# Kernel tuning notes

Hardware: AMD Instinct MI355X
Metric: run time of the kernel (lower is better)

The kernel has to match this reference:

```python
import jax, jax.numpy as jnp
import numpy as np

N_PROTS = 2048
MOLS_PER_PROT = 8
N_MOLS = N_PROTS * MOLS_PER_PROT
DIM = 768
MARGIN = 0.5


def setup_inputs() -> dict:
    key = jax.random.key(0)
    k1, k2, k3 = jax.random.split(key, 3)
    prot_emb = jax.random.normal(k1, (N_PROTS, DIM), dtype=jnp.float32)
    mol_emb = jax.random.normal(k2, (N_MOLS, DIM), dtype=jnp.float32)
    # L2-normalize like typical CLIP-style retrieval embeddings
    prot_emb = prot_emb / jnp.linalg.norm(prot_emb, axis=1, keepdims=True)
    mol_emb = mol_emb / jnp.linalg.norm(mol_emb, axis=1, keepdims=True)
    # block-structured labels: protein i paired with mols [8i, 8i+8)
    rows = jnp.repeat(jnp.arange(N_PROTS), MOLS_PER_PROT)
    cols = jnp.arange(N_MOLS)
    labels = jnp.zeros((N_PROTS, N_MOLS), dtype=jnp.float32).at[rows, cols].set(1.0)
    # pIC50 values in [2, 10]
    pic50_matrix = 2.0 + 8.0 * jax.random.uniform(k3, (N_PROTS, N_MOLS), dtype=jnp.float32)
    logit_scale = jnp.float32(1.0 / 0.07)
    return {"prot_emb": prot_emb, "mol_emb": mol_emb, "labels": labels,
            "pic50_matrix": pic50_matrix, "logit_scale": logit_scale}


def reference(prot_emb, mol_emb, labels, pic50_matrix, logit_scale):
    n_prots = prot_emb.shape[0]
    n_mols = mol_emb.shape[0]
    sim = jnp.matmul(prot_emb, mol_emb.T) * logit_scale  # [n_prots, n_mols]

    # affinity-weighted InfoNCE (prot -> mol)
    pic50_norm = jnp.clip((pic50_matrix - 2.0) / 8.0, 0.0, 1.0)
    pos_w = labels * pic50_norm
    pos_w = pos_w / (pos_w.sum(axis=1, keepdims=True) + 1e-8)
    loss_p2m = -jnp.sum(pos_w * jax.nn.log_softmax(sim, axis=1)) / n_prots

    # mol -> prot NLL
    mol_labels = jnp.argmax(labels, axis=0)  # [n_mols]
    lsm_m2p = jax.nn.log_softmax(sim.T, axis=1)  # [n_mols, n_prots]
    loss_m2p = -jnp.mean(lsm_m2p[jnp.arange(n_mols), mol_labels])

    # pairwise margin-ranking among positives (exactly MOLS_PER_PROT positives per protein)
    P = MOLS_PER_PROT
    _, pos_idx = jax.lax.top_k(labels, P)  # [n_prots, P] indices of positives
    pos_pic = jnp.take_along_axis(pic50_matrix, pos_idx, axis=1)  # [n_prots, P]
    pos_sc = jnp.take_along_axis(sim, pos_idx, axis=1)            # [n_prots, P]
    dp = pos_pic[:, :, None] - pos_pic[:, None, :]  # [n_prots, P, P]
    ds = pos_sc[:, :, None] - pos_sc[:, None, :]
    pair = jnp.where(dp > 0, jax.nn.relu(MARGIN - ds),
                     jnp.where(dp < 0, jax.nn.relu(MARGIN + ds), 0.0))
    upper = jnp.triu(jnp.ones((P, P), dtype=bool), k=1)  # unordered pairs j<k
    n_pairs = n_prots * (P * (P - 1) // 2)
    ranking_loss = jnp.sum(jnp.where(upper[None], pair, 0.0)) / n_pairs

    # negative push-down
    neg_loss = jnp.mean(jax.nn.relu(sim * (1.0 - labels)))

    total = loss_p2m + loss_m2p + 0.5 * ranking_loss + 0.1 * neg_loss
    return (total, loss_p2m, loss_m2p, ranking_loss, neg_loss)
```

## Files before the change

### kernel.cpp

```cpp
#include <hip/hip_runtime.h>
#include <hip/hip_bf16.h>
#include <math.h>

#define N_PROTS 2048
#define N_MOLS  16384
#define DIM     768
#define SHIFT   16.0f
#define MARGIN  0.5f

typedef __attribute__((ext_vector_type(8))) short short8;
typedef __attribute__((ext_vector_type(4))) float f32x4;
typedef __attribute__((ext_vector_type(4))) unsigned short us4;
typedef __attribute__((ext_vector_type(8))) unsigned short us8;

__device__ __forceinline__ unsigned short bf16rnd(float x) {
    unsigned int u = __float_as_uint(x);
    u += 0x7fffu + ((u >> 16) & 1u);
    return (unsigned short)(u >> 16);
}

__device__ __forceinline__ void gload16(const void* g, void* l) {
    __builtin_amdgcn_global_load_lds(
        (const __attribute__((address_space(1))) unsigned int*)g,
        (__attribute__((address_space(3))) unsigned int*)l, 16, 0, 0);
}

__device__ __forceinline__ int sig4(int x) { return (x + (x >> 2)) & 3; }

#define ACC_FLOATS 34824
#define PROT_BF_OFF_B 139296ull
#define PROT_BF_BYTES (2048ull*768*2)
#define MOL_BF_OFF_B  (PROT_BF_OFF_B + PROT_BF_BYTES)
#define MOL_BF_BYTES  (16384ull*768*2)
#define WS_NEED       (MOL_BF_OFF_B + MOL_BF_BYTES)

__global__ __launch_bounds__(256)
void convert_bf16(const float* __restrict__ prot, const float* __restrict__ mol,
                  unsigned short* __restrict__ protBf, unsigned short* __restrict__ molBf,
                  float* __restrict__ wsZero)
{
    const size_t PROT_G = (size_t)N_PROTS * DIM / 8;
    size_t t = (size_t)blockIdx.x * 256 + threadIdx.x;
    if (t < (ACC_FLOATS + 3) / 4) {
        float4 z = {0.f, 0.f, 0.f, 0.f};
        ((float4*)wsZero)[t] = z;
    }
    const float* src;
    unsigned short* dst;
    if (t < PROT_G) { src = prot + t * 8; dst = protBf + t * 8; }
    else            { size_t u = t - PROT_G; src = mol + u * 8; dst = molBf + u * 8; }
    float4 v0 = ((const float4*)src)[0];
    float4 v1 = ((const float4*)src)[1];
    us8 o;
    o[0] = bf16rnd(v0.x); o[1] = bf16rnd(v0.y); o[2] = bf16rnd(v0.z); o[3] = bf16rnd(v0.w);
    o[4] = bf16rnd(v1.x); o[5] = bf16rnd(v1.y); o[6] = bf16rnd(v1.z); o[7] = bf16rnd(v1.w);
    *(us8*)dst = o;
}

__global__ __launch_bounds__(512)
void sim_pass_bf16_v4(const unsigned short* __restrict__ protBf,
                      const unsigned short* __restrict__ molBf,
                      const float* __restrict__ scale_p,
                      float* __restrict__ row_se, float* __restrict__ col_se,
                      float* __restrict__ pos_sim, float* __restrict__ scalars)
{
    __shared__ unsigned short As[4][256][32];
    __shared__ unsigned short Bs[4][256][32];
    __shared__ float redBuf[8];

    const int tid = threadIdx.x;
    const int bid  = blockIdx.x;
    const int xcd  = bid & 7;
    const int sl8  = bid >> 3;
    const int bx   = xcd * 8 + (sl8 & 7);
    const int by   = sl8 >> 3;
    const int rowBase = by * 256;
    const int colBase = bx * 256;

    const int wave = tid >> 6;
    const int lane = tid & 63;
    const int wm = wave >> 2;
    const int wn = wave & 3;
    const int l15 = lane & 15;
    const int q   = lane >> 4;

    const int rsub = lane >> 2;
    const int cs   = lane & 3;
    const int csrc = (cs ^ sig4(rsub)) << 3;
    const unsigned short* aP =
        protBf + (size_t)(rowBase + wave * 32 + rsub) * DIM + csrc;
    const unsigned short* bP =
        molBf  + (size_t)(colBase + wave * 32 + rsub) * DIM + csrc;

#define STAGE_A(sl, ptr) do { \
    gload16((ptr),                     &As[sl][wave * 32][0]);      \
    gload16((ptr) + (size_t)16 * DIM,  &As[sl][wave * 32 + 16][0]); \
} while (0)
#define STAGE_B(sl, ptr) do { \
    gload16((ptr),                     &Bs[sl][wave * 32][0]);      \
    gload16((ptr) + (size_t)16 * DIM,  &Bs[sl][wave * 32 + 16][0]); \
} while (0)

    f32x4 acc[8][4];
#pragma unroll
    for (int i = 0; i < 8; ++i)
#pragma unroll
        for (int j = 0; j < 4; ++j) acc[i][j] = (f32x4){0.f, 0.f, 0.f, 0.f};

    STAGE_A(0, aP);      STAGE_B(0, bP);
    STAGE_A(1, aP + 32); STAGE_B(1, bP + 32);
    STAGE_A(2, aP + 64); STAGE_B(2, bP + 64);

    const int fArow = wm * 128 + l15;
    const int fBrow = wn * 64 + l15;
    const int fsw   = (q ^ sig4(l15)) << 3;

#pragma unroll 1
    for (int t = 0; t < 24; ++t) {
        const int sl = t & 3;
        const int pf = (t + 3) & 3;
        const int kt = (t < 21) ? (t + 3) : (t - 5);
        const unsigned short* aPt = aP + (size_t)kt * 32;
        const unsigned short* bPt = bP + (size_t)kt * 32;

        asm volatile("s_waitcnt vmcnt(8)" ::: "memory");
        __builtin_amdgcn_s_barrier();
        __builtin_amdgcn_sched_barrier(0);

        short8 aF[4], bF[4];
#pragma unroll
        for (int ni = 0; ni < 4; ++ni)
            bF[ni] = *(const short8*)&Bs[sl][fBrow + ni * 16][fsw];
#pragma unroll
        for (int mi = 0; mi < 4; ++mi)
            aF[mi] = *(const short8*)&As[sl][fArow + mi * 16][fsw];
        STAGE_A(pf, aPt);
        __builtin_amdgcn_s_setprio(1);
#pragma unroll
        for (int mi = 0; mi < 4; ++mi)
#pragma unroll
            for (int ni = 0; ni < 4; ++ni)
                acc[mi][ni] = __builtin_amdgcn_mfma_f32_16x16x32_bf16(
                    aF[mi], bF[ni], acc[mi][ni], 0, 0, 0);
        __builtin_amdgcn_s_setprio(0);

#pragma unroll
        for (int mi = 0; mi < 4; ++mi)
            aF[mi] = *(const short8*)&As[sl][fArow + 64 + mi * 16][fsw];
        STAGE_B(pf, bPt);
        __builtin_amdgcn_s_setprio(1);
#pragma unroll
        for (int mi = 0; mi < 4; ++mi)
#pragma unroll
            for (int ni = 0; ni < 4; ++ni)
                acc[4 + mi][ni] = __builtin_amdgcn_mfma_f32_16x16x32_bf16(
                    aF[mi], bF[ni], acc[4 + mi][ni], 0, 0, 0);
        __builtin_amdgcn_s_setprio(0);
    }
    asm volatile("s_waitcnt vmcnt(0)" ::: "memory");
#undef STAGE_A
#undef STAGE_B

    const float scale = scale_p[0];
    float csum[4] = {0.f, 0.f, 0.f, 0.f};
    float rl = 0.f;
#pragma unroll
    for (int mi = 0; mi < 8; ++mi) {
        float rs[4] = {0.f, 0.f, 0.f, 0.f};
#pragma unroll
        for (int ni = 0; ni < 4; ++ni) {
#pragma unroll
            for (int r = 0; r < 4; ++r) {
                float sim = acc[mi][ni][r] * scale;
                float e = __expf(sim - SHIFT);
                rs[r] += e;
                csum[ni] += e;
                rl += fmaxf(sim, 0.f);
                int rg = rowBase + wm * 128 + mi * 16 + q * 4 + r;
                int cg = colBase + wn * 64 + ni * 16 + l15;
                if ((cg >> 3) == rg) pos_sim[cg] = sim;
            }
        }
#pragma unroll
        for (int r = 0; r < 4; ++r) {
            float v = rs[r];
            v += __shfl_xor(v, 1); v += __shfl_xor(v, 2);
            v += __shfl_xor(v, 4); v += __shfl_xor(v, 8);
            if (l15 == 0)
                atomicAdd(&row_se[rowBase + wm * 128 + mi * 16 + q * 4 + r], v);
        }
    }
#pragma unroll
    for (int ni = 0; ni < 4; ++ni) {
        float v = csum[ni];
        v += __shfl_xor(v, 16); v += __shfl_xor(v, 32);
        if (q == 0)
            atomicAdd(&col_se[colBase + wn * 64 + ni * 16 + l15], v);
    }
#pragma unroll
    for (int m = 1; m < 64; m <<= 1) rl += __shfl_xor(rl, m);
    if (lane == 0) redBuf[wave] = rl;
    __syncthreads();
    if (tid == 0) {
        float sv = 0.f;
#pragma unroll
        for (int w = 0; w < 8; ++w) sv += redBuf[w];
        atomicAdd(&scalars[0], sv);
    }
}

__global__ __launch_bounds__(256, 2)
void sim_pass(const float* __restrict__ prot, const float* __restrict__ mol,
              const float* __restrict__ scale_p,
              float* __restrict__ row_se, float* __restrict__ col_se,
              float* __restrict__ pos_sim, float* __restrict__ scalars)
{
    __shared__ unsigned short As[128][32];
    __shared__ unsigned short Bs[128][32];
    __shared__ float redBuf[4];

    const int tid = threadIdx.x;
    const int rowBase = blockIdx.y * 128;
    const int colBase = blockIdx.x * 128;
    const int wave = tid >> 6;
    const int lane = tid & 63;
    const int wr = (wave >> 1) * 64;
    const int wc = (wave & 1) * 64;
    const int l15 = lane & 15;
    const int q   = lane >> 4;

    f32x4 acc[4][4];
#pragma unroll
    for (int i = 0; i < 4; ++i)
#pragma unroll
        for (int j = 0; j < 4; ++j) acc[i][j] = (f32x4){0.f, 0.f, 0.f, 0.f};

    const float* aBase = prot + (size_t)rowBase * DIM;
    const float* bBase = mol  + (size_t)colBase * DIM;
    float4 aReg[4], bReg[4];
#pragma unroll
    for (int i = 0; i < 4; ++i) {
        int f = tid + 256 * i;
        int row = f >> 3, c4 = f & 7;
        aReg[i] = *(const float4*)(aBase + (size_t)row * DIM + (c4 << 2));
        bReg[i] = *(const float4*)(bBase + (size_t)row * DIM + (c4 << 2));
    }
#pragma unroll 1
    for (int s = 0; s < DIM / 32; ++s) {
#pragma unroll
        for (int i = 0; i < 4; ++i) {
            int f = tid + 256 * i;
            int row = f >> 3, c4 = f & 7;
            us4 av, bv;
            av.x = bf16rnd(aReg[i].x); av.y = bf16rnd(aReg[i].y);
            av.z = bf16rnd(aReg[i].z); av.w = bf16rnd(aReg[i].w);
            bv.x = bf16rnd(bReg[i].x); bv.y = bf16rnd(bReg[i].y);
            bv.z = bf16rnd(bReg[i].z); bv.w = bf16rnd(bReg[i].w);
            *(us4*)&As[row][c4 << 2] = av;
            *(us4*)&Bs[row][c4 << 2] = bv;
        }
        __syncthreads();
        if (s + 1 < DIM / 32) {
            int k0 = (s + 1) * 32;
#pragma unroll
            for (int i = 0; i < 4; ++i) {
                int f = tid + 256 * i;
                int row = f >> 3, c4 = f & 7;
                aReg[i] = *(const float4*)(aBase + (size_t)row * DIM + k0 + (c4 << 2));
                bReg[i] = *(const float4*)(bBase + (size_t)row * DIM + k0 + (c4 << 2));
            }
        }
        short8 aF[4], bF[4];
#pragma unroll
        for (int mi = 0; mi < 4; ++mi) aF[mi] = *(const short8*)&As[wr + mi * 16 + l15][q * 8];
#pragma unroll
        for (int ni = 0; ni < 4; ++ni) bF[ni] = *(const short8*)&Bs[wc + ni * 16 + l15][q * 8];
#pragma unroll
        for (int mi = 0; mi < 4; ++mi)
#pragma unroll
            for (int ni = 0; ni < 4; ++ni)
                acc[mi][ni] = __builtin_amdgcn_mfma_f32_16x16x32_bf16(aF[mi], bF[ni], acc[mi][ni], 0, 0, 0);
        __syncthreads();
    }

    const float scale = scale_p[0];
    float rsum[4][4];
    float csum[4] = {0.f, 0.f, 0.f, 0.f};
    float rl = 0.f;
#pragma unroll
    for (int mi = 0; mi < 4; ++mi)
#pragma unroll
        for (int r = 0; r < 4; ++r) rsum[mi][r] = 0.f;
#pragma unroll
    for (int mi = 0; mi < 4; ++mi) {
#pragma unroll
        for (int ni = 0; ni < 4; ++ni) {
#pragma unroll
            for (int r = 0; r < 4; ++r) {
                float sim = acc[mi][ni][r] * scale;
                float e = __expf(sim - SHIFT);
                rsum[mi][r] += e;
                csum[ni] += e;
                rl += fmaxf(sim, 0.f);
                int rg = rowBase + wr + mi * 16 + q * 4 + r;
                int cg = colBase + wc + ni * 16 + l15;
                if ((cg >> 3) == rg) pos_sim[cg] = sim;
            }
        }
    }
#pragma unroll
    for (int mi = 0; mi < 4; ++mi) {
#pragma unroll
        for (int r = 0; r < 4; ++r) {
            float v = rsum[mi][r];
            v += __shfl_xor(v, 1); v += __shfl_xor(v, 2);
            v += __shfl_xor(v, 4); v += __shfl_xor(v, 8);
            if (l15 == 0)
                atomicAdd(&row_se[rowBase + wr + mi * 16 + q * 4 + r], v);
        }
    }
#pragma unroll
    for (int ni = 0; ni < 4; ++ni) {
        float v = csum[ni];
        v += __shfl_xor(v, 16); v += __shfl_xor(v, 32);
        if (q == 0)
            atomicAdd(&col_se[colBase + wc + ni * 16 + l15], v);
    }
#pragma unroll
    for (int m = 1; m < 64; m <<= 1) rl += __shfl_xor(rl, m);
    if (lane == 0) redBuf[wave] = rl;
    __syncthreads();
    if (tid == 0)
        atomicAdd(&scalars[0], redBuf[0] + redBuf[1] + redBuf[2] + redBuf[3]);
}

__global__ __launch_bounds__(256)
void finalize_mb(const float* __restrict__ row_se, const float* __restrict__ col_se,
                 const float* __restrict__ pos_sim, const float* __restrict__ pic50,
                 float* __restrict__ scalars, float* __restrict__ out)
{
    int j = blockIdx.x * 256 + threadIdx.x;
    float m2p = SHIFT + __logf(col_se[j]) - pos_sim[j];

    float p2m = 0.f, rank = 0.f, prelu = 0.f;
    if ((j & 7) == 0) {
        int i = j >> 3;
        float s[8], pc[8], pr[8];
#pragma unroll
        for (int p = 0; p < 8; ++p) {
            s[p]  = pos_sim[j + p];
            pr[p] = pic50[(size_t)i * N_MOLS + j + p];
            float x = (pr[p] - 2.0f) * 0.125f;
            pc[p] = fminf(fmaxf(x, 0.f), 1.f);
            prelu += fmaxf(s[p], 0.f);
        }
        float wsum = 1e-8f;
#pragma unroll
        for (int p = 0; p < 8; ++p) wsum += pc[p];
        float lse = SHIFT + __logf(row_se[i]);
        float accp = 0.f;
#pragma unroll
        for (int p = 0; p < 8; ++p) accp += pc[p] * (lse - s[p]);
        p2m = accp / wsum;
#pragma unroll
        for (int a = 0; a < 8; ++a)
#pragma unroll
            for (int b = a + 1; b < 8; ++b) {
                float dp = pr[a] - pr[b];
                float ds = s[a] - s[b];
                float v = (dp > 0.f) ? fmaxf(MARGIN - ds, 0.f)
                        : ((dp < 0.f) ? fmaxf(MARGIN + ds, 0.f) : 0.f);
                rank += v;
            }
    }

#pragma unroll
    for (int m = 1; m < 64; m <<= 1) {
        m2p   += __shfl_xor(m2p, m);
        p2m   += __shfl_xor(p2m, m);
        rank  += __shfl_xor(rank, m);
        prelu += __shfl_xor(prelu, m);
    }
    __shared__ float rbuf[4][4];
    const int wave = threadIdx.x >> 6, lane = threadIdx.x & 63;
    if (lane == 0) { rbuf[wave][0] = m2p; rbuf[wave][1] = p2m;
                     rbuf[wave][2] = rank; rbuf[wave][3] = prelu; }
    __syncthreads();
    if (threadIdx.x == 0) {
        float a = 0, b = 0, c = 0, d = 0;
        for (int w = 0; w < 4; ++w) { a += rbuf[w][0]; b += rbuf[w][1];
                                      c += rbuf[w][2]; d += rbuf[w][3]; }
        atomicAdd(&scalars[2], a);
        atomicAdd(&scalars[1], b);
        atomicAdd(&scalars[3], c);
        atomicAdd(&scalars[4], d);
        __threadfence();
        float old = atomicAdd(&scalars[7], 1.0f);
        if (old == (float)(N_MOLS / 256 - 1)) {
            float s0 = atomicAdd(&scalars[0], 0.0f);
            float s1 = atomicAdd(&scalars[1], 0.0f);
            float s2 = atomicAdd(&scalars[2], 0.0f);
            float s3 = atomicAdd(&scalars[3], 0.0f);
            float s4 = atomicAdd(&scalars[4], 0.0f);
            float relu_neg = s0 - s4;
            float p2mv  = s1 / (float)N_PROTS;
            float m2pv  = s2 / (float)N_MOLS;
            float rankv = s3 / ((float)N_PROTS * 28.0f);
            float negv  = relu_neg / ((float)N_PROTS * (float)N_MOLS);
            out[0] = p2mv + m2pv + 0.5f * rankv + 0.1f * negv;
            out[1] = p2mv;
            out[2] = m2pv;
            out[3] = rankv;
            out[4] = negv;
        }
    }
}

extern "C" void kernel_launch(void* const* d_in, const int* in_sizes, int n_in,
                              void* d_out, int out_size, void* d_ws, size_t ws_size,
                              hipStream_t stream) {
    const float* prot   = (const float*)d_in[0];
    const float* mol    = (const float*)d_in[1];
    const float* pic50  = (const float*)d_in[3];
    const float* lscale = (const float*)d_in[4];

    float* ws      = (float*)d_ws;
    float* row_se  = ws;
    float* col_se  = ws + 2048;
    float* pos_sim = ws + 2048 + 16384;
    float* scalars = ws + 2048 + 16384 + 16384;

    if (ws_size >= WS_NEED) {
        unsigned short* protBf = (unsigned short*)((char*)d_ws + PROT_BF_OFF_B);
        unsigned short* molBf  = (unsigned short*)((char*)d_ws + MOL_BF_OFF_B);
        size_t groups = ((size_t)N_PROTS + N_MOLS) * DIM / 8;
        convert_bf16<<<(unsigned)(groups / 256), 256, 0, stream>>>(prot, mol, protBf, molBf, ws);
        sim_pass_bf16_v4<<<512, 512, 0, stream>>>(protBf, molBf, lscale, row_se, col_se, pos_sim, scalars);
    } else {
        hipMemsetAsync(d_ws, 0, (size_t)ACC_FLOATS * sizeof(float), stream);
        dim3 grid(N_MOLS / 128, N_PROTS / 128);
        sim_pass<<<grid, 256, 0, stream>>>(prot, mol, lscale, row_se, col_se, pos_sim, scalars);
    }
    finalize_mb<<<N_MOLS / 256, 256, 0, stream>>>(row_se, col_se, pos_sim, pic50, scalars, (float*)d_out);
}
```

Before: 376.8 us.

## Fuse bf16 conversion, GEMM and finalize into one persistent kernel

Replaces the separate convert, bf16 sim-pass and finalize launches with one persistent kernel of 256 blocks. Each block first converts a strided slice of the embeddings to bf16 and joins a grid-wide atomic barrier, then computes two 256x256 similarity tiles. The last block to finish, detected with an atomic ticket, runs the final loss reduction. This removes two launch boundaries and the extra zeroing pass. In exchange it depends on all 256 blocks being resident at once for the spin barrier, halves the block count, and puts the whole finalize on a single block.

Measured after the change: 527.1 us. +39.9%, slower.

```diff
diff --git a/kernel.cpp b/kernel.cpp
--- a/kernel.cpp
+++ b/kernel.cpp
@@ -26,6 +26,10 @@
 }
 
 __device__ __forceinline__ int sig4(int x) { return (x + (x >> 2)) & 3; }
+
+__device__ __forceinline__ float aload(const float* p) {
+    return __hip_atomic_load(p, __ATOMIC_RELAXED, __HIP_MEMORY_SCOPE_AGENT);
+}
 
 #define ACC_FLOATS 34824
 #define PROT_BF_OFF_B 139296ull
@@ -34,48 +38,65 @@
 #define MOL_BF_BYTES  (16384ull*768*2)
 #define WS_NEED       (MOL_BF_OFF_B + MOL_BF_BYTES)
 
-__global__ __launch_bounds__(256)
-void convert_bf16(const float* __restrict__ prot, const float* __restrict__ mol,
-                  unsigned short* __restrict__ protBf, unsigned short* __restrict__ molBf,
-                  float* __restrict__ wsZero)
-{
-    const size_t PROT_G = (size_t)N_PROTS * DIM / 8;
-    size_t t = (size_t)blockIdx.x * 256 + threadIdx.x;
-    if (t < (ACC_FLOATS + 3) / 4) {
-        float4 z = {0.f, 0.f, 0.f, 0.f};
-        ((float4*)wsZero)[t] = z;
-    }
-    const float* src;
-    unsigned short* dst;
-    if (t < PROT_G) { src = prot + t * 8; dst = protBf + t * 8; }
-    else            { size_t u = t - PROT_G; src = mol + u * 8; dst = molBf + u * 8; }
-    float4 v0 = ((const float4*)src)[0];
-    float4 v1 = ((const float4*)src)[1];
-    us8 o;
-    o[0] = bf16rnd(v0.x); o[1] = bf16rnd(v0.y); o[2] = bf16rnd(v0.z); o[3] = bf16rnd(v0.w);
-    o[4] = bf16rnd(v1.x); o[5] = bf16rnd(v1.y); o[6] = bf16rnd(v1.z); o[7] = bf16rnd(v1.w);
-    *(us8*)dst = o;
-}
+#define GROUPS  ((size_t)(N_PROTS + N_MOLS) * DIM / 8)
+#define PROT_G  ((size_t)N_PROTS * DIM / 8)
 
 __global__ __launch_bounds__(512)
-void sim_pass_bf16_v4(const unsigned short* __restrict__ protBf,
-                      const unsigned short* __restrict__ molBf,
-                      const float* __restrict__ scale_p,
-                      float* __restrict__ row_se, float* __restrict__ col_se,
-                      float* __restrict__ pos_sim, float* __restrict__ scalars)
+void fused_all(const float* __restrict__ prot, const float* __restrict__ mol,
+               const float* __restrict__ pic50, const float* __restrict__ scale_p,
+               unsigned short* __restrict__ protBf, unsigned short* __restrict__ molBf,
+               float* __restrict__ wsBase, float* __restrict__ out)
 {
     __shared__ unsigned short As[4][256][32];
     __shared__ unsigned short Bs[4][256][32];
     __shared__ float redBuf[8];
+    __shared__ float rbuf2[8][4];
+    __shared__ unsigned int winnerFlag;
+
+    float* row_se  = wsBase;
+    float* col_se  = wsBase + 2048;
+    float* pos_sim = wsBase + 2048 + 16384;
+    float* scalars = wsBase + 34816;
+    unsigned int* bar  = (unsigned int*)(scalars + 5);
+    unsigned int* tick = (unsigned int*)(scalars + 6);
 
     const int tid = threadIdx.x;
-    const int bid  = blockIdx.x;
-    const int xcd  = bid & 7;
-    const int sl8  = bid >> 3;
-    const int bx   = xcd * 8 + (sl8 & 7);
-    const int by   = sl8 >> 3;
-    const int rowBase = by * 256;
-    const int colBase = bx * 256;
+    const int bid = blockIdx.x;
+    const size_t lin = (size_t)bid * 512 + tid;
+
+    if (lin < 8704) {
+        float4 z = {0.f, 0.f, 0.f, 0.f};
+        ((float4*)wsBase)[lin] = z;
+    }
+    for (size_t g = lin; g < GROUPS; g += (size_t)256 * 512) {
+        const float* src;
+        unsigned short* dst;
+        if (g < PROT_G) { src = prot + g * 8; dst = protBf + g * 8; }
+        else            { size_t u = g - PROT_G; src = mol + u * 8; dst = molBf + u * 8; }
+        float4 v0 = ((const float4*)src)[0];
+        float4 v1 = ((const float4*)src)[1];
+        us8 o;
+        o[0] = bf16rnd(v0.x); o[1] = bf16rnd(v0.y); o[2] = bf16rnd(v0.z); o[3] = bf16rnd(v0.w);
+        o[4] = bf16rnd(v1.x); o[5] = bf16rnd(v1.y); o[6] = bf16rnd(v1.z); o[7] = bf16rnd(v1.w);
+        *(us8*)dst = o;
+    }
+
+    __threadfence();
+    __syncthreads();
+    if (tid == 0) {
+        __hip_atomic_fetch_add(bar, 1u, __ATOMIC_ACQ_REL, __HIP_MEMORY_SCOPE_AGENT);
+        unsigned int spins = 0;
+        while (__hip_atomic_load(bar, __ATOMIC_ACQUIRE, __HIP_MEMORY_SCOPE_AGENT) < 256u) {
+            __builtin_amdgcn_s_sleep(1);
+            if (++spins > 200000000u) break;
+        }
+    }
+    __syncthreads();
+
+    const int xcd = bid & 7;
+    const int s   = bid >> 3;
+    const int by  = s >> 2;
+    const int bxh = xcd * 4 + (s & 3);
 
     const int wave = tid >> 6;
     const int lane = tid & 63;
@@ -87,10 +108,14 @@
     const int rsub = lane >> 2;
     const int cs   = lane & 3;
     const int csrc = (cs ^ sig4(rsub)) << 3;
-    const unsigned short* aP =
-        protBf + (size_t)(rowBase + wave * 32 + rsub) * DIM + csrc;
-    const unsigned short* bP =
-        molBf  + (size_t)(colBase + wave * 32 + rsub) * DIM + csrc;
+
+    const int fArow = wm * 128 + l15;
+    const int fBrow = wn * 64 + l15;
+    const int fsw   = (q ^ sig4(l15)) << 3;
+
+    const float scale = scale_p[0];
+    const int rowBase = by * 256;
+    float rl = 0.f;
 
 #define STAGE_A(sl, ptr) do { \
     gload16((ptr),                     &As[sl][wave * 32][0]);      \
@@ -101,102 +126,107 @@
     gload16((ptr) + (size_t)16 * DIM,  &Bs[sl][wave * 32 + 16][0]); \
 } while (0)
 
-    f32x4 acc[8][4];
-#pragma unroll
-    for (int i = 0; i < 8; ++i)
-#pragma unroll
-        for (int j = 0; j < 4; ++j) acc[i][j] = (f32x4){0.f, 0.f, 0.f, 0.f};
-
-    STAGE_A(0, aP);      STAGE_B(0, bP);
-    STAGE_A(1, aP + 32); STAGE_B(1, bP + 32);
-    STAGE_A(2, aP + 64); STAGE_B(2, bP + 64);
-
-    const int fArow = wm * 128 + l15;
-    const int fBrow = wn * 64 + l15;
-    const int fsw   = (q ^ sig4(l15)) << 3;
-
 #pragma unroll 1
-    for (int t = 0; t < 24; ++t) {
-        const int sl = t & 3;
-        const int pf = (t + 3) & 3;
-        const int kt = (t < 21) ? (t + 3) : (t - 5);
-        const unsigned short* aPt = aP + (size_t)kt * 32;
-        const unsigned short* bPt = bP + (size_t)kt * 32;
-
-        asm volatile("s_waitcnt vmcnt(8)" ::: "memory");
-        __builtin_amdgcn_s_barrier();
-        __builtin_amdgcn_sched_barrier(0);
-
-        short8 aF[4], bF[4];
-#pragma unroll
-        for (int ni = 0; ni < 4; ++ni)
-            bF[ni] = *(const short8*)&Bs[sl][fBrow + ni * 16][fsw];
-#pragma unroll
-        for (int mi = 0; mi < 4; ++mi)
-            aF[mi] = *(const short8*)&As[sl][fArow + mi * 16][fsw];
-        STAGE_A(pf, aPt);
-        __builtin_amdgcn_s_setprio(1);
-#pragma unroll
-        for (int mi = 0; mi < 4; ++mi)
+    for (int ct = 0; ct < 2; ++ct) {
+        const int colBase = (2 * bxh + ct) * 256;
+        const unsigned short* aP =
+            protBf + (size_t)(rowBase + wave * 32 + rsub) * DIM + csrc;
+        const unsigned short* bP =
+            molBf  + (size_t)(colBase + wave * 32 + rsub) * DIM + csrc;
+
+        f32x4 acc[8][4];
+#pragma unroll
+        for (int i = 0; i < 8; ++i)
+#pragma unroll
+            for (int j = 0; j < 4; ++j) acc[i][j] = (f32x4){0.f, 0.f, 0.f, 0.f};
+
+        STAGE_A(0, aP);      STAGE_B(0, bP);
+        STAGE_A(1, aP + 32); STAGE_B(1, bP + 32);
+        STAGE_A(2, aP + 64); STAGE_B(2, bP + 64);
+
+#pragma unroll 1
+        for (int t = 0; t < 24; ++t) {
+            const int sl = t & 3;
+            const int pf = (t + 3) & 3;
+            const int kt = (t < 21) ? (t + 3) : (t - 5);
+            const unsigned short* aPt = aP + (size_t)kt * 32;
+            const unsigned short* bPt = bP + (size_t)kt * 32;
+
+            asm volatile("s_waitcnt vmcnt(8)" ::: "memory");
+            __builtin_amdgcn_s_barrier();
+            __builtin_amdgcn_sched_barrier(0);
+
+            short8 aF[4], bF[4];
 #pragma unroll
             for (int ni = 0; ni < 4; ++ni)
-                acc[mi][ni] = __builtin_amdgcn_mfma_f32_16x16x32_bf16(
-                    aF[mi], bF[ni], acc[mi][ni], 0, 0, 0);
-        __builtin_amdgcn_s_setprio(0);
-
-#pragma unroll
-        for (int mi = 0; mi < 4; ++mi)
-            aF[mi] = *(const short8*)&As[sl][fArow + 64 + mi * 16][fsw];
-        STAGE_B(pf, bPt);
-        __builtin_amdgcn_s_setprio(1);
-#pragma unroll
-        for (int mi = 0; mi < 4; ++mi)
-#pragma unroll
-            for (int ni = 0; ni < 4; ++ni)
-                acc[4 + mi][ni] = __builtin_amdgcn_mfma_f32_16x16x32_bf16(
-                    aF[mi], bF[ni], acc[4 + mi][ni], 0, 0, 0);
-        __builtin_amdgcn_s_setprio(0);
-    }
-    asm volatile("s_waitcnt vmcnt(0)" ::: "memory");
+                bF[ni] = *(const short8*)&Bs[sl][fBrow + ni * 16][fsw];
+#pragma unroll
+            for (int mi = 0; mi < 4; ++mi)
+                aF[mi] = *(const short8*)&As[sl][fArow + mi * 16][fsw];
+            STAGE_A(pf, aPt);
+            __builtin_amdgcn_s_setprio(1);
+#pragma unroll
+            for (int mi = 0; mi < 4; ++mi)
+#pragma unroll
+                for (int ni = 0; ni < 4; ++ni)
+                    acc[mi][ni] = __builtin_amdgcn_mfma_f32_16x16x32_bf16(
+                        aF[mi], bF[ni], acc[mi][ni], 0, 0, 0);
+            __builtin_amdgcn_s_setprio(0);
+
+#pragma unroll
+            for (int mi = 0; mi < 4; ++mi)
+                aF[mi] = *(const short8*)&As[sl][fArow + 64 + mi * 16][fsw];
+            STAGE_B(pf, bPt);
+            __builtin_amdgcn_s_setprio(1);
+#pragma unroll
+            for (int mi = 0; mi < 4; ++mi)
+#pragma unroll
+                for (int ni = 0; ni < 4; ++ni)
+                    acc[4 + mi][ni] = __builtin_amdgcn_mfma_f32_16x16x32_bf16(
+                        aF[mi], bF[ni], acc[4 + mi][ni], 0, 0, 0);
+            __builtin_amdgcn_s_setprio(0);
+        }
+        asm volatile("s_waitcnt vmcnt(0)" ::: "memory");
+
+        float csum[4] = {0.f, 0.f, 0.f, 0.f};
+#pragma unroll
+        for (int mi = 0; mi < 8; ++mi) {
+            float rs[4] = {0.f, 0.f, 0.f, 0.f};
+#pragma unroll
+            for (int ni = 0; ni < 4; ++ni) {
+#pragma unroll
+                for (int r = 0; r < 4; ++r) {
+                    float sim = acc[mi][ni][r] * scale;
+                    float e = __expf(sim - SHIFT);
+                    rs[r] += e;
+                    csum[ni] += e;
+                    rl += fmaxf(sim, 0.f);
+                    int rg = rowBase + wm * 128 + mi * 16 + q * 4 + r;
+                    int cg = colBase + wn * 64 + ni * 16 + l15;
+                    if ((cg >> 3) == rg) pos_sim[cg] = sim;
+                }
+            }
+#pragma unroll
+            for (int r = 0; r < 4; ++r) {
+                float v = rs[r];
+                v += __shfl_xor(v, 1); v += __shfl_xor(v, 2);
+                v += __shfl_xor(v, 4); v += __shfl_xor(v, 8);
+                if (l15 == 0)
+                    atomicAdd(&row_se[rowBase + wm * 128 + mi * 16 + q * 4 + r], v);
+            }
+        }
+#pragma unroll
+        for (int ni = 0; ni < 4; ++ni) {
+            float v = csum[ni];
+            v += __shfl_xor(v, 16); v += __shfl_xor(v, 32);
+            if (q == 0)
+                atomicAdd(&col_se[colBase + wn * 64 + ni * 16 + l15], v);
+        }
+        __syncthreads();
+    }
 #undef STAGE_A
 #undef STAGE_B
 
-    const float scale = scale_p[0];
-    float csum[4] = {0.f, 0.f, 0.f, 0.f};
-    float rl = 0.f;
-#pragma unroll
-    for (int mi = 0; mi < 8; ++mi) {
-        float rs[4] = {0.f, 0.f, 0.f, 0.f};
-#pragma unroll
-        for (int ni = 0; ni < 4; ++ni) {
-#pragma unroll
-            for (int r = 0; r < 4; ++r) {
-                float sim = acc[mi][ni][r] * scale;
-                float e = __expf(sim - SHIFT);
-                rs[r] += e;
-                csum[ni] += e;
-                rl += fmaxf(sim, 0.f);
-                int rg = rowBase + wm * 128 + mi * 16 + q * 4 + r;
-                int cg = colBase + wn * 64 + ni * 16 + l15;
-                if ((cg >> 3) == rg) pos_sim[cg] = sim;
-            }
-        }
-#pragma unroll
-        for (int r = 0; r < 4; ++r) {
-            float v = rs[r];
-            v += __shfl_xor(v, 1); v += __shfl_xor(v, 2);
-            v += __shfl_xor(v, 4); v += __shfl_xor(v, 8);
-            if (l15 == 0)
-                atomicAdd(&row_se[rowBase + wm * 128 + mi * 16 + q * 4 + r], v);
-        }
-    }
-#pragma unroll
-    for (int ni = 0; ni < 4; ++ni) {
-        float v = csum[ni];
-        v += __shfl_xor(v, 16); v += __shfl_xor(v, 32);
-        if (q == 0)
-            atomicAdd(&col_se[colBase + wn * 64 + ni * 16 + l15], v);
-    }
 #pragma unroll
     for (int m = 1; m < 64; m <<= 1) rl += __shfl_xor(rl, m);
     if (lane == 0) redBuf[wave] = rl;
@@ -206,6 +236,79 @@
 #pragma unroll
         for (int w = 0; w < 8; ++w) sv += redBuf[w];
         atomicAdd(&scalars[0], sv);
+    }
+
+    __threadfence();
+    __syncthreads();
+    if (tid == 0) {
+        unsigned int old = __hip_atomic_fetch_add(tick, 1u, __ATOMIC_ACQ_REL,
+                                                  __HIP_MEMORY_SCOPE_AGENT);
+        winnerFlag = (old == 255u) ? 1u : 0u;
+    }
+    __syncthreads();
+    if (!winnerFlag) return;
+
+    float m2p = 0.f, p2m = 0.f, rank = 0.f, prelu = 0.f;
+    for (int j = tid; j < N_MOLS; j += 512) {
+        float cse = aload(&col_se[j]);
+        float ps  = aload(&pos_sim[j]);
+        m2p += SHIFT + __logf(cse) - ps;
+    }
+    for (int i = tid; i < N_PROTS; i += 512) {
+        const int j0 = i << 3;
+        float sarr[8], pc[8], pr[8];
+#pragma unroll
+        for (int p = 0; p < 8; ++p) {
+            sarr[p] = aload(&pos_sim[j0 + p]);
+            pr[p]   = pic50[(size_t)i * N_MOLS + j0 + p];
+            float x = (pr[p] - 2.0f) * 0.125f;
+            pc[p] = fminf(fmaxf(x, 0.f), 1.f);
+            prelu += fmaxf(sarr[p], 0.f);
+        }
+        float wsum = 1e-8f;
+#pragma unroll
+        for (int p = 0; p < 8; ++p) wsum += pc[p];
+        float lse = SHIFT + __logf(aload(&row_se[i]));
+        float accp = 0.f;
+#pragma unroll
+        for (int p = 0; p < 8; ++p) accp += pc[p] * (lse - sarr[p]);
+        p2m += accp / wsum;
+#pragma unroll
+        for (int a = 0; a < 8; ++a)
+#pragma unroll
+            for (int b = a + 1; b < 8; ++b) {
+                float dp = pr[a] - pr[b];
+                float ds = sarr[a] - sarr[b];
+                float v = (dp > 0.f) ? fmaxf(MARGIN - ds, 0.f)
+                        : ((dp < 0.f) ? fmaxf(MARGIN + ds, 0.f) : 0.f);
+                rank += v;
+            }
+    }
+#pragma unroll
+    for (int m = 1; m < 64; m <<= 1) {
+        m2p   += __shfl_xor(m2p, m);
+        p2m   += __shfl_xor(p2m, m);
+        rank  += __shfl_xor(rank, m);
+        prelu += __shfl_xor(prelu, m);
+    }
+    if (lane == 0) { rbuf2[wave][0] = m2p; rbuf2[wave][1] = p2m;
+                     rbuf2[wave][2] = rank; rbuf2[wave][3] = prelu; }
+    __syncthreads();
+    if (tid == 0) {
+        float a = 0, b = 0, c = 0, d = 0;
+        for (int w = 0; w < 8; ++w) { a += rbuf2[w][0]; b += rbuf2[w][1];
+                                      c += rbuf2[w][2]; d += rbuf2[w][3]; }
+        float s0 = aload(&scalars[0]);
+        float relu_neg = s0 - d;
+        float p2mv  = b / (float)N_PROTS;
+        float m2pv  = a / (float)N_MOLS;
+        float rankv = c / ((float)N_PROTS * 28.0f);
+        float negv  = relu_neg / ((float)N_PROTS * (float)N_MOLS);
+        out[0] = p2mv + m2pv + 0.5f * rankv + 0.1f * negv;
+        out[1] = p2mv;
+        out[2] = m2pv;
+        out[3] = rankv;
+        out[4] = negv;
     }
 }
 
@@ -373,7 +476,6 @@
                 rank += v;
             }
     }
-
 #pragma unroll
     for (int m = 1; m < 64; m <<= 1) {
         m2p   += __shfl_xor(m2p, m);
@@ -425,21 +527,21 @@
     const float* lscale = (const float*)d_in[4];
 
     float* ws      = (float*)d_ws;
-    float* row_se  = ws;
-    float* col_se  = ws + 2048;
-    float* pos_sim = ws + 2048 + 16384;
-    float* scalars = ws + 2048 + 16384 + 16384;
+    float* scalars = ws + 34816;
 
     if (ws_size >= WS_NEED) {
         unsigned short* protBf = (unsigned short*)((char*)d_ws + PROT_BF_OFF_B);
         unsigned short* molBf  = (unsigned short*)((char*)d_ws + MOL_BF_OFF_B);
-        size_t groups = ((size_t)N_PROTS + N_MOLS) * DIM / 8;
-        convert_bf16<<<(unsigned)(groups / 256), 256, 0, stream>>>(prot, mol, protBf, molBf, ws);
-        sim_pass_bf16_v4<<<512, 512, 0, stream>>>(protBf, molBf, lscale, row_se, col_se, pos_sim, scalars);
+        hipMemsetAsync(scalars, 0, 8 * sizeof(float), stream);
+        fused_all<<<256, 512, 0, stream>>>(prot, mol, pic50, lscale,
+                                           protBf, molBf, ws, (float*)d_out);
     } else {
         hipMemsetAsync(d_ws, 0, (size_t)ACC_FLOATS * sizeof(float), stream);
+        float* row_se  = ws;
+        float* col_se  = ws + 2048;
+        float* pos_sim = ws + 2048 + 16384;
         dim3 grid(N_MOLS / 128, N_PROTS / 128);
         sim_pass<<<grid, 256, 0, stream>>>(prot, mol, lscale, row_se, col_se, pos_sim, scalars);
-    }
-    finalize_mb<<<N_MOLS / 256, 256, 0, stream>>>(row_se, col_se, pos_sim, pic50, scalars, (float*)d_out);
-}
+        finalize_mb<<<N_MOLS / 256, 256, 0, stream>>>(row_se, col_se, pos_sim, pic50, scalars, (float*)d_out);
+    }
+}
```
